# Kernel optimization log

Measured on AMD Instinct MI355X. Metric: run time of the kernel, lower is better.

The kernel has to match this reference:

```python
import math
import jax, jax.numpy as jnp
import numpy as np

# model config (matches init_kwargs)
V, D, DC, DM, DE, DG, H, L, TMAX = 32000, 1024, 512, 1024, 4096, 1024, 16, 6, 2048
CHD = max(1, DC // H)   # q/k head dim = 32
MHD = max(1, DM // H)   # v head dim   = 64
B, T = 2, 1024
EPS = 1e-5


def setup_inputs() -> dict:
    key = jax.random.key(0)
    ks = iter(jax.random.split(key, 40))
    s = 0.02
    rn = lambda shape: jax.random.normal(next(ks), shape, dtype=jnp.float32) * s
    inp = {
        'ids': jax.random.randint(next(ks), (B, T), 0, V),
        'te': rn((V, D)),            # tied token embedding / lm head weight
        'pe': rn((TMAX, D)),
        # per-layer stacked params, leading dim L
        'ln1_g': jnp.ones((L, D)), 'ln1_b': jnp.zeros((L, D)),
        'qp_w': rn((L, D, H * CHD)), 'qp_b': jnp.zeros((L, H * CHD)),
        'kp_w': rn((L, D, H * CHD)), 'kp_b': jnp.zeros((L, H * CHD)),
        'vp_w': rn((L, D, H * MHD)), 'vp_b': jnp.zeros((L, H * MHD)),
        'out_w': rn((L, H * MHD, D)), 'out_b': jnp.zeros((L, D)),
        'ln2_g': jnp.ones((L, D)), 'ln2_b': jnp.zeros((L, D)),
        'exp_w': rn((L, D, DE)), 'exp_b': jnp.zeros((L, DE)),
        'gate_w': rn((L, D, DG)), 'gate_b': jnp.zeros((L, DG)),
        'gup_w': rn((L, DG, DE)), 'gup_b': jnp.zeros((L, DE)),
        'comp_w': rn((L, DE, D)), 'comp_b': jnp.zeros((L, D)),
        'lnf_g': jnp.ones((D,)), 'lnf_b': jnp.zeros((D,)),
    }
    return inp


def _ln(x, g, b):
    m = jnp.mean(x, axis=-1, keepdims=True)
    v = jnp.mean(jnp.square(x - m), axis=-1, keepdims=True)
    return (x - m) * jax.lax.rsqrt(v + EPS) * g + b


def _forward(ids, te, pe, ln1_g, ln1_b, qp_w, qp_b, kp_w, kp_b, vp_w, vp_b,
             out_w, out_b, ln2_g, ln2_b, exp_w, exp_b, gate_w, gate_b,
             gup_w, gup_b, comp_w, comp_b, lnf_g, lnf_b):
    b, t = ids.shape
    x = te[ids] + pe[jnp.arange(t)][None, :, :]          # [B,T,D]
    causal = jnp.tril(jnp.ones((t, t), dtype=bool))       # [T,T]
    scale = 1.0 / math.sqrt(CHD)

    def block(x, p):
        (l1g, l1b, qw, qb, kw, kb, vw, vb, ow, ob,
         l2g, l2b, ew, eb, gw, gb, guw, gub, cw, cb) = p
        # --- attention sublayer ---
        h = _ln(x, l1g, l1b)
        q = (h @ qw + qb).reshape(b, t, H, CHD)
        k = (h @ kw + kb).reshape(b, t, H, CHD)
        v = (h @ vw + vb).reshape(b, t, H, MHD)
        sc = jnp.einsum('bqhd,bkhd->bhqk', q, k) * scale
        sc = jnp.where(causal[None, None], sc, -jnp.inf)
        a = jax.nn.softmax(sc, axis=-1)
        y = jnp.einsum('bhqk,bkhd->bqhd', a, v).reshape(b, t, H * MHD)
        x = x + y @ ow + ob
        # --- gated FFN sublayer ---
        h2 = _ln(x, l2g, l2b)
        e = h2 @ ew + eb
        g = jax.nn.sigmoid(jax.nn.silu(h2 @ gw + gb) @ guw + gub)
        x = x + jax.nn.silu(e * g) @ cw + cb
        return x, None

    params = (ln1_g, ln1_b, qp_w, qp_b, kp_w, kp_b, vp_w, vp_b, out_w, out_b,
              ln2_g, ln2_b, exp_w, exp_b, gate_w, gate_b, gup_w, gup_b,
              comp_w, comp_b)
    x, _ = jax.lax.scan(block, x, params)
    logits = _ln(x, lnf_g, lnf_b) @ te.T                  # tied head, [B,T,V]
    return logits


def reference(ids, te, pe, ln1_g, ln1_b, qp_w, qp_b, kp_w, kp_b, vp_w, vp_b,
              out_w, out_b, ln2_g, ln2_b, exp_w, exp_b, gate_w, gate_b,
              gup_w, gup_b, comp_w, comp_b, lnf_g, lnf_b):
    return _forward(ids, te, pe, ln1_g, ln1_b, qp_w, qp_b, kp_w, kp_b,
                    vp_w, vp_b, out_w, out_b, ln2_g, ln2_b, exp_w, exp_b,
                    gate_w, gate_b, gup_w, gup_b, comp_w, comp_b,
                    lnf_g, lnf_b)
```

## Files before the change

kernel.cpp:

```cpp
#include <hip/hip_runtime.h>
#include <math.h>

typedef unsigned short u16;
typedef unsigned int   u32;
typedef __attribute__((ext_vector_type(4))) float f32x4;
typedef __attribute__((ext_vector_type(8))) short s16x8;

#define D_   1024
#define DE_  4096
#define H_   16
#define CHD_ 32
#define MHD_ 64
#define L_   6
#define B_   2
#define T_   1024
#define M_   (B_*T_)
#define V_   32000
#define EPS_ 1e-5f

__device__ __forceinline__ float bf2f(u16 u){ return __uint_as_float(((u32)u) << 16); }
__device__ __forceinline__ u16 f2bf(float f){
    u32 x = __float_as_uint(f);
    return (u16)((x + 0x7fffu + ((x >> 16) & 1u)) >> 16);
}
__device__ __forceinline__ float ldf(const void* p, size_t i, int f16){
    return f16 ? bf2f(((const u16*)p)[i]) : ((const float*)p)[i];
}
__device__ __forceinline__ float sigf(float x){ return 1.f / (1.f + __expf(-x)); }

typedef __attribute__((address_space(3))) u32 as3_u32;
typedef const __attribute__((address_space(1))) u32 as1_u32;
__device__ __forceinline__ void gld16(const void* g, void* l){
    __builtin_amdgcn_global_load_lds((as1_u32*)g, (as3_u32*)l, 16, 0, 0);
}
__device__ __forceinline__ int swz(int row){ return (row >> 1) & 3; }

__global__ void detect_dtype(const u16* __restrict__ te_u16, int* __restrict__ flag){
    __shared__ int any_big;
    if (threadIdx.x == 0) any_big = 0;
    __syncthreads();
    int big = 0;
    #pragma unroll
    for (int i=0;i<4;i++){
        u16 u = te_u16[threadIdx.x + 256*i];
        int e = (u >> 7) & 0xFF;
        if (e >= 0x88) big = 1;
    }
    if (big) any_big = 1;
    __syncthreads();
    if (threadIdx.x == 0) *flag = any_big ? 0 : 1;
}

__global__ __launch_bounds__(256) void conv_te(const void* __restrict__ te,
        u16* __restrict__ dst, const int* __restrict__ flagp){
    int f16 = *flagp;
    size_t i = ((size_t)blockIdx.x*256 + threadIdx.x)*8;
    if (f16){
        *(s16x8*)(dst+i) = *(const s16x8*)((const u16*)te + i);
    } else {
        const float* s = (const float*)te + i;
        float4 f0 = *(const float4*)s, f1 = *(const float4*)(s+4);
        s16x8 pk;
        pk[0]=(short)f2bf(f0.x); pk[1]=(short)f2bf(f0.y);
        pk[2]=(short)f2bf(f0.z); pk[3]=(short)f2bf(f0.w);
        pk[4]=(short)f2bf(f1.x); pk[5]=(short)f2bf(f1.y);
        pk[6]=(short)f2bf(f1.z); pk[7]=(short)f2bf(f1.w);
        *(s16x8*)(dst+i) = pk;
    }
}

__global__ __launch_bounds__(256) void embed_kernel(const int* __restrict__ ids,
        const void* __restrict__ te, const void* __restrict__ pe,
        float* __restrict__ x, const int* __restrict__ flagp){
    int f16 = *flagp;
    int idx = blockIdx.x*256 + threadIdx.x;
    int m = idx >> 10, d = idx & 1023;
    int t = m & (T_-1);
    x[idx] = ldf(te, (size_t)ids[m]*D_ + d, f16) + ldf(pe, (size_t)t*D_ + d, f16);
}

__device__ __forceinline__ float blk_sum(float v, float* smem){
    #pragma unroll
    for (int o=32;o>0;o>>=1) v += __shfl_xor(v, o);
    __syncthreads();
    if ((threadIdx.x & 63) == 0) smem[threadIdx.x>>6] = v;
    __syncthreads();
    return smem[0]+smem[1]+smem[2]+smem[3];
}

__global__ __launch_bounds__(256) void ln_kernel(const float* __restrict__ x,
        const void* __restrict__ g, const void* __restrict__ b, size_t goff,
        u16* __restrict__ out, const int* __restrict__ flagp){
    __shared__ float smem[4];
    int f16 = *flagp;
    int row = blockIdx.x, tid = threadIdx.x;
    const float* xr = x + (size_t)row*D_;
    float v[4]; float s = 0.f;
    #pragma unroll
    for (int i=0;i<4;i++){ v[i] = xr[tid+256*i]; s += v[i]; }
    float mean = blk_sum(s, smem) * (1.f/D_);
    float vs = 0.f;
    #pragma unroll
    for (int i=0;i<4;i++){ float d = v[i]-mean; vs += d*d; }
    float inv = rsqrtf(blk_sum(vs, smem)*(1.f/D_) + EPS_);
    u16* orow = out + (size_t)row*D_;
    #pragma unroll
    for (int i=0;i<4;i++){
        int c = tid+256*i;
        orow[c] = f2bf((v[i]-mean)*inv*ldf(g, goff+c, f16) + ldf(b, goff+c, f16));
    }
}

__global__ __launch_bounds__(256) void wt_tr(
        const void* s0, size_t o0, u16* d0,
        const void* s1, size_t o1, u16* d1,
        const void* s2, size_t o2, u16* d2,
        int K, int N, const int* __restrict__ flagp){
    const void* s; size_t o; u16* d;
    if (blockIdx.z == 0){ s=s0; o=o0; d=d0; }
    else if (blockIdx.z == 1){ s=s1; o=o1; d=d1; }
    else { s=s2; o=o2; d=d2; }
    int f16 = *flagp;
    __shared__ float tile[64][65];
    int k0 = blockIdx.y*64, n0 = blockIdx.x*64;
    int t = threadIdx.x;
    if (!f16){
        int c4 = (t & 15)*4, r = t >> 4;
        const float* S = (const float*)s + o + (size_t)(k0 + r)*N + n0 + c4;
        #pragma unroll
        for (int i=0;i<4;i++){
            float4 v = *(const float4*)(S + (size_t)(16*i)*N);
            tile[r+16*i][c4+0] = v.x; tile[r+16*i][c4+1] = v.y;
            tile[r+16*i][c4+2] = v.z; tile[r+16*i][c4+3] = v.w;
        }
    } else {
        int c = t & 63, r4 = t >> 6;
        #pragma unroll
        for (int i=0;i<16;i++){
            int r = r4 + i*4;
            tile[r][c] = bf2f(((const u16*)s)[o + (size_t)(k0+r)*N + n0 + c]);
        }
    }
    __syncthreads();
    int n = t >> 2, kq = (t & 3)*16;
    s16x8 lo, hi;
    #pragma unroll
    for (int i=0;i<8;i++) lo[i] = (short)f2bf(tile[kq+i][n]);
    #pragma unroll
    for (int i=0;i<8;i++) hi[i] = (short)f2bf(tile[kq+8+i][n]);
    u16* D = d + (size_t)(n0+n)*K + k0 + kq;
    *(s16x8*)D = lo;
    *(s16x8*)(D+8) = hi;
}

__global__ __launch_bounds__(256) void v_transpose(const u16* __restrict__ qkv,
                                                   u16* __restrict__ vt){
    __shared__ u16 tile[32][34];
    int bh = blockIdx.z, b = bh >> 4, h = bh & 15;
    int t0 = blockIdx.x*32, d0 = blockIdx.y*32;
    int c = threadIdx.x & 31, r8 = threadIdx.x >> 5;
    #pragma unroll
    for (int i=0;i<4;i++){
        int r = r8 + i*8;
        tile[r][c] = qkv[(size_t)(b*T_ + t0 + r)*2048 + 1024 + h*64 + d0 + c];
    }
    __syncthreads();
    #pragma unroll
    for (int i=0;i<4;i++){
        int r = r8 + i*8;
        vt[(size_t)(bh*64 + d0 + r)*T_ + t0 + c] = tile[c][r];
    }
}

__global__ __launch_bounds__(256) void bias_cat(
        const void* qb_, const void* kb_, const void* vb_,
        const void* eb_, const void* gb_,
        size_t oq, size_t ok, size_t ov, size_t oe, size_t og,
        float* __restrict__ b1, float* __restrict__ b2,
        const int* __restrict__ flagp){
    int f16 = *flagp;
    int i = blockIdx.x*256 + threadIdx.x;
    if (i < 2048){
        float v = (i < 512)  ? ldf(qb_, oq + i, f16)
                : (i < 1024) ? ldf(kb_, ok + i - 512, f16)
                :              ldf(vb_, ov + i - 1024, f16);
        b1[i] = v;
    } else {
        int j = i - 2048;
        float v = (j < DE_) ? ldf(eb_, oe + j, f16)
                            : ldf(gb_, og + j - DE_, f16);
        b2[j] = v;
    }
}

template<int MODE, bool RESID, bool BIASF32, int TN, int SK>
__global__ __launch_bounds__(256) void gemm_mfma(
        const u16* __restrict__ A, int lda,
        const void* __restrict__ B, int ldb,
        const void* __restrict__ bias, size_t boff,
        void* __restrict__ C, int ldc,
        int N, int K, const int* __restrict__ flagp){
    constexpr int MT = (TN == 128) ? 4 : 2;
    constexpr int NT = 4;
    constexpr int BCALLS = TN / 32;
    __shared__ __align__(16) char smem[16384 + TN*128];
    char* ldsA = smem;
    char* ldsB = smem + 16384;
    const int t = threadIdx.x;
    const int w = t >> 6, lane = t & 63;
    const int fr = lane & 15, g = lane >> 4;
    const int wm = (TN == 128) ? (w >> 1) * 64 : w * 32;
    const int wn = (TN == 128) ? (w & 1) * 64 : 0;

    const int gx = gridDim.x, gy = gridDim.y;
    const int nwg = gx * gy;
    const int lin = blockIdx.y * gx + blockIdx.x;
    const int neu = (lin & 7) * (nwg >> 3) + (lin >> 3);
    const int m0 = (neu % gy) * 128;
    const int n0 = (neu / gy) * TN;

    const int f16 = *flagp;
    const bool convB = (MODE == 3) && !f16;

    const int srow = t >> 3, sslot = t & 7;
    const u16* srcA   = A + (size_t)(m0 + srow) * lda + 8 * (sslot ^ (srow & 7));
    const u16* srcB16 = (const u16*)B + (size_t)(n0 + srow) * ldb + 8 * (sslot ^ (srow & 7));
    const int crow = t >> 1, chalf = t & 1;
    const float* srcBf = (const float*)B + (size_t)(n0 + crow) * ldb;

    char* dstA = ldsA + w * 1024;
    char* dstB = ldsB + w * 1024;

    f32x4 acc[MT][NT];
    const f32x4 zero = {0.f, 0.f, 0.f, 0.f};
    #pragma unroll
    for (int i=0;i<MT;i++)
        #pragma unroll
        for (int j=0;j<NT;j++) acc[i][j] = zero;

    const int kps  = K / SK;
    const int kbeg = (SK > 1) ? blockIdx.z * kps : 0;
    const int kend = kbeg + kps;

    for (int k0 = kbeg; k0 < kend; k0 += 64){
        #pragma unroll
        for (int i=0;i<4;i++)
            gld16(srcA + (size_t)(32*i)*lda + k0, dstA + i*4096);
        if (!convB){
            #pragma unroll
            for (int i=0;i<BCALLS;i++)
                gld16(srcB16 + (size_t)(32*i)*ldb + k0, dstB + i*4096);
        } else {
            #pragma unroll
            for (int s4=0;s4<4;s4++){
                int sl = chalf*4 + s4;
                const float* sp = srcBf + k0 + 8*(sl ^ (crow & 7));
                float4 f0 = *(const float4*)sp;
                float4 f1 = *(const float4*)(sp + 4);
                s16x8 pk;
                pk[0]=(short)f2bf(f0.x); pk[1]=(short)f2bf(f0.y);
                pk[2]=(short)f2bf(f0.z); pk[3]=(short)f2bf(f0.w);
                pk[4]=(short)f2bf(f1.x); pk[5]=(short)f2bf(f1.y);
                pk[6]=(short)f2bf(f1.z); pk[7]=(short)f2bf(f1.w);
                *(s16x8*)(ldsB + crow*128 + sl*16) = pk;
            }
        }
        __syncthreads();
        #pragma unroll
        for (int kk=0;kk<2;kk++){
            const int so = ((kk*4 + g) ^ (fr & 7)) * 16;
            s16x8 a[MT], b[NT];
            #pragma unroll
            for (int mt=0;mt<MT;mt++)
                a[mt] = *(const s16x8*)(ldsA + (wm + mt*16 + fr)*128 + so);
            #pragma unroll
            for (int nt=0;nt<NT;nt++)
                b[nt] = *(const s16x8*)(ldsB + (wn + nt*16 + fr)*128 + so);
            #pragma unroll
            for (int mt=0;mt<MT;mt++)
                #pragma unroll
                for (int nt=0;nt<NT;nt++)
                    acc[mt][nt] = __builtin_amdgcn_mfma_f32_16x16x32_bf16(
                                      a[mt], b[nt], acc[mt][nt], 0, 0, 0);
        }
        __syncthreads();
    }

    const bool addb = (SK == 1) || (blockIdx.z == 0);
    #pragma unroll
    for (int nt=0;nt<NT;nt++){
        const int nc = n0 + wn + nt*16 + fr;
        float bv = 0.f;
        if (MODE != 3 && MODE != 5 && addb)
            bv = BIASF32 ? ((const float*)bias)[boff + nc]
                         : ldf(bias, boff + nc, f16);
        #pragma unroll
        for (int mt=0;mt<MT;mt++){
            #pragma unroll
            for (int r=0;r<4;r++){
                const int mr = m0 + wm + mt*16 + g*4 + r;
                const size_t idx = (size_t)mr * ldc + nc;
                float val = acc[mt][nt][r] + bv;
                if (MODE == 4){
                    if (nc >= DE_) val = val * sigf(val);
                    ((u16*)C)[idx] = f2bf(val);
                } else if (MODE == 2){
                    float e = bf2f(((const u16*)C)[idx]);
                    float z = e * sigf(val);
                    ((u16*)C)[idx] = f2bf(z * sigf(z));
                } else if (MODE == 3 || MODE == 5){
                    if (f16) ((u16*)C)[idx] = f2bf(val);
                    else     ((float*)C)[idx] = val;
                } else if (RESID){
                    if (SK > 1) unsafeAtomicAdd(&((float*)C)[idx], val);
                    else        ((float*)C)[idx] += val;
                } else {
                    ((u16*)C)[idx] = f2bf(val);
                }
            }
        }
    }
}

__global__ __launch_bounds__(256) void attn_mfma(const u16* __restrict__ qkv,
                                                 const u16* __restrict__ vt,
                                                 u16* __restrict__ y){
    __shared__ __align__(16) char smem[21504];
    char* ldsK = smem;
    char* ldsV = smem + 4096;
    char* ldsP = smem + 12288;

    const int qt = gridDim.x - 1 - blockIdx.x;
    const int h = blockIdx.y, b = blockIdx.z;
    const int t = threadIdx.x, w = t >> 6, lane = t & 63;
    const int fr = lane & 15, g = lane >> 4;
    const int q0 = qt * 64;
    const int qw = q0 + w * 16;
    const int bh = b * H_ + h;

    const int srow = t >> 2, sslot = t & 3;
    const u16* srcK = qkv + (size_t)(b*T_ + srow)*2048 + 512 + h*32
                      + 8 * (sslot ^ swz(srow));
    const int vrow = t >> 3, vslot = t & 7;
    const u16* srcV0 = vt + (size_t)(bh*64 + vrow)*T_      + 8 * (vslot ^ (vrow & 7));
    const u16* srcV1 = vt + (size_t)(bh*64 + 32 + vrow)*T_ + 8 * (vslot ^ (vrow & 7));

    s16x8 qf = *(const s16x8*)(qkv + (size_t)(b*T_ + qw + fr)*2048 + h*32 + g*8);

    char* pbase = ldsP + w * 2304;

    f32x4 o[4]; float m[4], l[4];
    #pragma unroll
    for (int f=0; f<4; f++) o[f] = (f32x4){0.f,0.f,0.f,0.f};
    #pragma unroll
    for (int r=0; r<4; r++){ m[r] = -3.0e38f; l[r] = 0.f; }

    const float scale = 0.17677669529663687f;
    const f32x4 zero = {0.f,0.f,0.f,0.f};

    for (int j0 = 0; j0 < q0 + 64; j0 += 64){
        __syncthreads();
        gld16(srcK + (size_t)j0*2048, ldsK + w*1024);
        gld16(srcV0 + j0,             ldsV + w*1024);
        gld16(srcV1 + j0,             ldsV + 4096 + w*1024);
        __syncthreads();
        if (j0 <= qw + 15){
            f32x4 s[4];
            #pragma unroll
            for (int f=0; f<4; f++){
                int row = f*16 + fr;
                s16x8 kf = *(const s16x8*)(ldsK + row*64 + (g ^ swz(row))*16);
                s[f] = __builtin_amdgcn_mfma_f32_16x16x32_bf16(qf, kf, zero, 0,0,0);
            }
            bool needmask = (j0 + 63 > qw);
            #pragma unroll
            for (int f=0; f<4; f++){
                int j = j0 + f*16 + fr;
                #pragma unroll
                for (int r=0; r<4; r++){
                    float sv = s[f][r] * scale;
                    if (needmask && j > qw + g*4 + r) sv = -3.0e38f;
                    s[f][r] = sv;
                }
            }
            float mx[4];
            #pragma unroll
            for (int r=0; r<4; r++)
                mx[r] = fmaxf(fmaxf(s[0][r], s[1][r]), fmaxf(s[2][r], s[3][r]));
            #pragma unroll
            for (int o2=8; o2>0; o2>>=1)
                #pragma unroll
                for (int r=0; r<4; r++) mx[r] = fmaxf(mx[r], __shfl_xor(mx[r], o2));
            float al[4];
            #pragma unroll
            for (int r=0; r<4; r++){
                float mn = fmaxf(m[r], mx[r]);
                al[r] = __expf(m[r] - mn);
                m[r] = mn;
            }
            float ps[4] = {0.f,0.f,0.f,0.f};
            #pragma unroll
            for (int f=0; f<4; f++)
                #pragma unroll
                for (int r=0; r<4; r++){
                    float p = __expf(s[f][r] - m[r]);
                    ps[r] += p;
                    *(u16*)(pbase + (g*4+r)*144 + (fr + 16*f)*2) = f2bf(p);
                }
            #pragma unroll
            for (int o2=8; o2>0; o2>>=1)
                #pragma unroll
                for (int r=0; r<4; r++) ps[r] += __shfl_xor(ps[r], o2);
            #pragma unroll
            for (int r=0; r<4; r++) l[r] = l[r]*al[r] + ps[r];
            #pragma unroll
            for (int f=0; f<4; f++)
                #pragma unroll
                for (int r=0; r<4; r++) o[f][r] *= al[r];
            #pragma unroll
            for (int kk=0; kk<2; kk++){
                s16x8 pa = *(const s16x8*)(pbase + fr*144 + kk*64 + g*16);
                #pragma unroll
                for (int f=0; f<4; f++){
                    int row = f*16 + fr;
                    s16x8 vb = *(const s16x8*)(ldsV + row*128 + (((kk*4+g) ^ (row&7))*16));
                    o[f] = __builtin_amdgcn_mfma_f32_16x16x32_bf16(pa, vb, o[f], 0,0,0);
                }
            }
        }
    }
    #pragma unroll
    for (int r=0; r<4; r++){
        float inv = 1.f / l[r];
        u16* yr = y + (size_t)(b*T_ + qw + g*4 + r)*1024 + h*64;
        #pragma unroll
        for (int f=0; f<4; f++)
            yr[fr + 16*f] = f2bf(o[f][r] * inv);
    }
}

extern "C" void kernel_launch(void* const* d_in, const int* in_sizes, int n_in,
                              void* d_out, int out_size, void* d_ws, size_t ws_size,
                              hipStream_t stream){
    const int*  ids   = (const int*) d_in[0];
    const void* te    = d_in[1];
    const void* pe    = d_in[2];
    const void* ln1_g = d_in[3];
    const void* ln1_b = d_in[4];
    const void* qp_w  = d_in[5];
    const void* qp_b  = d_in[6];
    const void* kp_w  = d_in[7];
    const void* kp_b  = d_in[8];
    const void* vp_w  = d_in[9];
    const void* vp_b  = d_in[10];
    const void* out_w = d_in[11];
    const void* out_b = d_in[12];
    const void* ln2_g = d_in[13];
    const void* ln2_b = d_in[14];
    const void* exp_w = d_in[15];
    const void* exp_b = d_in[16];
    const void* gate_w= d_in[17];
    const void* gate_b= d_in[18];
    const void* gup_w = d_in[19];
    const void* gup_b = d_in[20];
    const void* comp_w= d_in[21];
    const void* comp_b= d_in[22];
    const void* lnf_g = d_in[23];
    const void* lnf_b = d_in[24];

    char* ws = (char*)d_ws;
    int*   flag  = (int*)ws;
    float* bcat1 = (float*)(ws + 4096);
    float* bcat2 = (float*)(ws + 4096 + 8192);
    float* x     = (float*)(ws + (1u<<20));
    u16*   hb    = (u16*)  (ws + (9u<<20));
    u16*   qkvb  = (u16*)  (ws + (13u<<20));
    u16*   yb    = (u16*)  (ws + (21u<<20));
    u16*   vtb   = (u16*)  (ws + (25u<<20));
    u16*   eg1   = (u16*)  (ws + (13u<<20));
    u16*   wb    = (u16*)  (ws + (33u<<20));
    u16*   te16  = (u16*)  (ws + ((size_t)44<<20));

    const size_t need = ((size_t)44<<20) + (size_t)V_*D_*2 + (1u<<20);
    const bool pre = (ws_size >= need);

    detect_dtype<<<1, 256, 0, stream>>>((const u16*)te, flag);
    if (pre)
        conv_te<<<(V_*D_)/2048, 256, 0, stream>>>(te, te16, flag);
    embed_kernel<<<(M_*D_)/256, 256, 0, stream>>>(ids, te, pe, x, flag);

    for (int l=0; l<L_; l++){
        size_t lD = (size_t)l*D_;
        wt_tr<<<dim3(8,16,2), 256, 0, stream>>>(
            qp_w, (size_t)l*D_*512, wb,
            kp_w, (size_t)l*D_*512, wb + (size_t)512*1024,
            nullptr, 0, nullptr, 1024, 512, flag);
        wt_tr<<<dim3(16,16,2), 256, 0, stream>>>(
            vp_w,  (size_t)l*D_*1024,  wb + (size_t)1024*1024,
            out_w, (size_t)l*1024*1024, wb + (size_t)2048*1024,
            nullptr, 0, nullptr, 1024, 1024, flag);
        bias_cat<<<28, 256, 0, stream>>>(qp_b, kp_b, vp_b, exp_b, gate_b,
            (size_t)l*512, (size_t)l*512, (size_t)l*1024,
            (size_t)l*DE_, (size_t)l*1024, bcat1, bcat2, flag);

        ln_kernel<<<M_, 256, 0, stream>>>(x, ln1_g, ln1_b, lD, hb, flag);
        gemm_mfma<0,false,true,64,1><<<dim3(32,16), 256, 0, stream>>>(
            hb, 1024, wb, 1024, bcat1, 0, qkvb, 2048, 2048, 1024, flag);
        v_transpose<<<dim3(32,2,32), 256, 0, stream>>>(qkvb, vtb);
        attn_mfma<<<dim3(T_/64, H_, B_), 256, 0, stream>>>(qkvb, vtb, yb);
        gemm_mfma<0,true,false,64,2><<<dim3(16,16,2), 256, 0, stream>>>(
            yb, 1024, wb + (size_t)2048*1024, 1024,
            out_b, (size_t)l*1024, x, 1024, 1024, 1024, flag);

        wt_tr<<<dim3(64,16,1), 256, 0, stream>>>(
            exp_w, (size_t)l*D_*DE_, wb,
            nullptr,0,nullptr, nullptr,0,nullptr, 1024, 4096, flag);
        wt_tr<<<dim3(16,16,1), 256, 0, stream>>>(
            gate_w, (size_t)l*D_*1024, wb + (size_t)4096*1024,
            nullptr,0,nullptr, nullptr,0,nullptr, 1024, 1024, flag);
        ln_kernel<<<M_, 256, 0, stream>>>(x, ln2_g, ln2_b, lD, hb, flag);
        gemm_mfma<4,false,true,128,1><<<dim3(40,16), 256, 0, stream>>>(
            hb, 1024, wb, 1024, bcat2, 0, eg1, 5120, 5120, 1024, flag);
        wt_tr<<<dim3(64,16,1), 256, 0, stream>>>(
            gup_w, (size_t)l*1024*DE_, wb,
            nullptr,0,nullptr, nullptr,0,nullptr, 1024, 4096, flag);
        gemm_mfma<2,false,false,128,1><<<dim3(32,16), 256, 0, stream>>>(
            eg1 + 4096, 5120, wb, 1024,
            gup_b, (size_t)l*DE_, eg1, 5120, 4096, 1024, flag);
        wt_tr<<<dim3(16,64,1), 256, 0, stream>>>(
            comp_w, (size_t)l*DE_*1024, wb,
            nullptr,0,nullptr, nullptr,0,nullptr, 4096, 1024, flag);
        gemm_mfma<0,true,false,64,2><<<dim3(16,16,2), 256, 0, stream>>>(
            eg1, 5120, wb, 4096, comp_b, (size_t)l*1024, x, 1024, 1024, 4096, flag);
    }

    ln_kernel<<<M_, 256, 0, stream>>>(x, lnf_g, lnf_b, 0, hb, flag);
    if (pre)
        gemm_mfma<5,false,false,128,1><<<dim3(V_/128, M_/128), 256, 0, stream>>>(
            hb, 1024, te16, 1024, nullptr, 0, d_out, V_, V_, 1024, flag);
    else
        gemm_mfma<3,false,false,128,1><<<dim3(V_/128, M_/128), 256, 0, stream>>>(
            hb, 1024, te, 1024, nullptr, 0, d_out, V_, V_, 1024, flag);
}
```

Measured before the change: 2.170 ms.

## Double-buffer LDS tiles in GEMM and attention kernels with async prefetch

```diff
diff --git a/kernel.cpp b/kernel.cpp
--- a/kernel.cpp
+++ b/kernel.cpp
@@ -30,8 +30,21 @@
 
 typedef __attribute__((address_space(3))) u32 as3_u32;
 typedef const __attribute__((address_space(1))) u32 as1_u32;
+typedef __attribute__((address_space(3))) const char as3c;
 __device__ __forceinline__ void gld16(const void* g, void* l){
     __builtin_amdgcn_global_load_lds((as1_u32*)g, (as3_u32*)l, 16, 0, 0);
+}
+__device__ __forceinline__ s16x8 dsr(const char* p){
+    s16x8 v;
+    u32 off = (u32)(size_t)(as3c*)p;
+    asm volatile("ds_read_b128 %0, %1" : "=v"(v) : "v"(off));
+    return v;
+}
+#define LGKM0()  asm volatile("s_waitcnt lgkmcnt(0)" ::: "memory")
+#define SCHED0() __builtin_amdgcn_sched_barrier(0)
+#define SBAR()   __builtin_amdgcn_s_barrier()
+template<int N> __device__ __forceinline__ void vmwait(){
+    asm volatile("s_waitcnt vmcnt(%0)" :: "n"(N) : "memory");
 }
 __device__ __forceinline__ int swz(int row){ return (row >> 1) & 3; }
 
@@ -193,19 +206,28 @@
     }
 }
 
+template<int BC>
+__device__ __forceinline__ void stage_ab(const u16* sA, const u16* sB,
+        int lda, int ldb, char* dA, char* dB, int k0){
+    #pragma unroll
+    for (int i=0;i<4;i++)  gld16(sA + (size_t)(32*i)*lda + k0, dA + i*4096);
+    #pragma unroll
+    for (int i=0;i<BC;i++) gld16(sB + (size_t)(32*i)*ldb + k0, dB + i*4096);
+}
+
 template<int MODE, bool RESID, bool BIASF32, int TN, int SK>
-__global__ __launch_bounds__(256) void gemm_mfma(
+__global__ __launch_bounds__(256) void gemm_pipe(
         const u16* __restrict__ A, int lda,
-        const void* __restrict__ B, int ldb,
+        const u16* __restrict__ B, int ldb,
         const void* __restrict__ bias, size_t boff,
         void* __restrict__ C, int ldc,
         int N, int K, const int* __restrict__ flagp){
     constexpr int MT = (TN == 128) ? 4 : 2;
     constexpr int NT = 4;
-    constexpr int BCALLS = TN / 32;
-    __shared__ __align__(16) char smem[16384 + TN*128];
-    char* ldsA = smem;
-    char* ldsB = smem + 16384;
+    constexpr int BC = TN / 32;
+    constexpr int L  = 4 + BC;
+    constexpr int BUFSZ = 16384 + TN*128;
+    __shared__ __align__(16) char smem[2*BUFSZ];
     const int t = threadIdx.x;
     const int w = t >> 6, lane = t & 63;
     const int fr = lane & 15, g = lane >> 4;
@@ -220,36 +242,132 @@
     const int n0 = (neu / gy) * TN;
 
     const int f16 = *flagp;
-    const bool convB = (MODE == 3) && !f16;
 
     const int srow = t >> 3, sslot = t & 7;
-    const u16* srcA   = A + (size_t)(m0 + srow) * lda + 8 * (sslot ^ (srow & 7));
+    const u16* srcA = A + (size_t)(m0 + srow) * lda + 8 * (sslot ^ (srow & 7));
+    const u16* srcB = B + (size_t)(n0 + srow) * ldb + 8 * (sslot ^ (srow & 7));
+
+    f32x4 acc[MT][NT];
+    #pragma unroll
+    for (int i=0;i<MT;i++)
+        #pragma unroll
+        for (int j=0;j<NT;j++) acc[i][j] = (f32x4){0.f,0.f,0.f,0.f};
+
+    const int kps  = K / SK;
+    const int kbeg = (SK > 1) ? blockIdx.z * kps : 0;
+    const int nt_  = kps >> 6;
+
+    stage_ab<BC>(srcA, srcB, lda, ldb,
+                 smem + w*1024, smem + 16384 + w*1024, kbeg);
+    for (int it=0; it<nt_; ++it){
+        const int cur = it & 1;
+        if (it+1 < nt_){
+            const int nb = cur^1;
+            stage_ab<BC>(srcA, srcB, lda, ldb,
+                         smem + nb*BUFSZ + w*1024,
+                         smem + nb*BUFSZ + 16384 + w*1024,
+                         kbeg + (it+1)*64);
+            vmwait<L>();
+        } else {
+            vmwait<0>();
+        }
+        SBAR();
+        const char* bA = smem + cur*BUFSZ;
+        const char* bB = smem + cur*BUFSZ + 16384;
+        #pragma unroll
+        for (int kk=0;kk<2;kk++){
+            const int so = ((kk*4 + g) ^ (fr & 7)) * 16;
+            s16x8 a[MT], b[NT];
+            #pragma unroll
+            for (int mt=0;mt<MT;mt++)
+                a[mt] = dsr(bA + (wm + mt*16 + fr)*128 + so);
+            #pragma unroll
+            for (int n2=0;n2<NT;n2++)
+                b[n2] = dsr(bB + (wn + n2*16 + fr)*128 + so);
+            LGKM0(); SCHED0();
+            #pragma unroll
+            for (int mt=0;mt<MT;mt++)
+                #pragma unroll
+                for (int n2=0;n2<NT;n2++)
+                    acc[mt][n2] = __builtin_amdgcn_mfma_f32_16x16x32_bf16(
+                                      a[mt], b[n2], acc[mt][n2], 0, 0, 0);
+        }
+        SBAR();
+    }
+
+    const bool addb = (SK == 1) || (blockIdx.z == 0);
+    #pragma unroll
+    for (int n2=0;n2<NT;n2++){
+        const int nc = n0 + wn + n2*16 + fr;
+        float bv = 0.f;
+        if (MODE != 5 && addb)
+            bv = BIASF32 ? ((const float*)bias)[boff + nc]
+                         : ldf(bias, boff + nc, f16);
+        #pragma unroll
+        for (int mt=0;mt<MT;mt++){
+            #pragma unroll
+            for (int r=0;r<4;r++){
+                const int mr = m0 + wm + mt*16 + g*4 + r;
+                const size_t idx = (size_t)mr * ldc + nc;
+                float val = acc[mt][n2][r] + bv;
+                if (MODE == 4){
+                    if (nc >= DE_) val = val * sigf(val);
+                    ((u16*)C)[idx] = f2bf(val);
+                } else if (MODE == 2){
+                    float e = bf2f(((const u16*)C)[idx]);
+                    float z = e * sigf(val);
+                    ((u16*)C)[idx] = f2bf(z * sigf(z));
+                } else if (MODE == 5){
+                    if (f16) ((u16*)C)[idx] = f2bf(val);
+                    else     ((float*)C)[idx] = val;
+                } else if (RESID){
+                    if (SK > 1) unsafeAtomicAdd(&((float*)C)[idx], val);
+                    else        ((float*)C)[idx] += val;
+                } else {
+                    ((u16*)C)[idx] = f2bf(val);
+                }
+            }
+        }
+    }
+}
+
+__global__ __launch_bounds__(256) void gemm_head_f32(
+        const u16* __restrict__ A, int lda,
+        const void* __restrict__ B, int ldb,
+        void* __restrict__ C, int ldc,
+        int N, int K, const int* __restrict__ flagp){
+    __shared__ __align__(16) char smem[16384 + 16384];
+    char* ldsA = smem;
+    char* ldsB = smem + 16384;
+    const int t = threadIdx.x;
+    const int w = t >> 6, lane = t & 63;
+    const int fr = lane & 15, g = lane >> 4;
+    const int wm = (w >> 1) * 64, wn = (w & 1) * 64;
+    const int gx = gridDim.x, gy = gridDim.y;
+    const int nwg = gx * gy;
+    const int lin = blockIdx.y * gx + blockIdx.x;
+    const int neu = (lin & 7) * (nwg >> 3) + (lin >> 3);
+    const int m0 = (neu % gy) * 128;
+    const int n0 = (neu / gy) * 128;
+    const int f16 = *flagp;
+    const int srow = t >> 3, sslot = t & 7;
+    const u16* srcA = A + (size_t)(m0 + srow) * lda + 8 * (sslot ^ (srow & 7));
     const u16* srcB16 = (const u16*)B + (size_t)(n0 + srow) * ldb + 8 * (sslot ^ (srow & 7));
     const int crow = t >> 1, chalf = t & 1;
     const float* srcBf = (const float*)B + (size_t)(n0 + crow) * ldb;
-
-    char* dstA = ldsA + w * 1024;
-    char* dstB = ldsB + w * 1024;
-
-    f32x4 acc[MT][NT];
-    const f32x4 zero = {0.f, 0.f, 0.f, 0.f};
-    #pragma unroll
-    for (int i=0;i<MT;i++)
-        #pragma unroll
-        for (int j=0;j<NT;j++) acc[i][j] = zero;
-
-    const int kps  = K / SK;
-    const int kbeg = (SK > 1) ? blockIdx.z * kps : 0;
-    const int kend = kbeg + kps;
-
-    for (int k0 = kbeg; k0 < kend; k0 += 64){
+    f32x4 acc[4][4];
+    #pragma unroll
+    for (int i=0;i<4;i++)
+        #pragma unroll
+        for (int j=0;j<4;j++) acc[i][j] = (f32x4){0.f,0.f,0.f,0.f};
+    for (int k0 = 0; k0 < K; k0 += 64){
         #pragma unroll
         for (int i=0;i<4;i++)
-            gld16(srcA + (size_t)(32*i)*lda + k0, dstA + i*4096);
-        if (!convB){
-            #pragma unroll
-            for (int i=0;i<BCALLS;i++)
-                gld16(srcB16 + (size_t)(32*i)*ldb + k0, dstB + i*4096);
+            gld16(srcA + (size_t)(32*i)*lda + k0, ldsA + w*1024 + i*4096);
+        if (f16){
+            #pragma unroll
+            for (int i=0;i<4;i++)
+                gld16(srcB16 + (size_t)(32*i)*ldb + k0, ldsB + w*1024 + i*4096);
         } else {
             #pragma unroll
             for (int s4=0;s4<4;s4++){
@@ -269,54 +387,33 @@
         #pragma unroll
         for (int kk=0;kk<2;kk++){
             const int so = ((kk*4 + g) ^ (fr & 7)) * 16;
-            s16x8 a[MT], b[NT];
-            #pragma unroll
-            for (int mt=0;mt<MT;mt++)
+            s16x8 a[4], b[4];
+            #pragma unroll
+            for (int mt=0;mt<4;mt++)
                 a[mt] = *(const s16x8*)(ldsA + (wm + mt*16 + fr)*128 + so);
             #pragma unroll
-            for (int nt=0;nt<NT;nt++)
+            for (int nt=0;nt<4;nt++)
                 b[nt] = *(const s16x8*)(ldsB + (wn + nt*16 + fr)*128 + so);
             #pragma unroll
-            for (int mt=0;mt<MT;mt++)
-                #pragma unroll
-                for (int nt=0;nt<NT;nt++)
+            for (int mt=0;mt<4;mt++)
+                #pragma unroll
+                for (int nt=0;nt<4;nt++)
                     acc[mt][nt] = __builtin_amdgcn_mfma_f32_16x16x32_bf16(
                                       a[mt], b[nt], acc[mt][nt], 0, 0, 0);
         }
         __syncthreads();
     }
-
-    const bool addb = (SK == 1) || (blockIdx.z == 0);
-    #pragma unroll
-    for (int nt=0;nt<NT;nt++){
+    #pragma unroll
+    for (int nt=0;nt<4;nt++){
         const int nc = n0 + wn + nt*16 + fr;
-        float bv = 0.f;
-        if (MODE != 3 && MODE != 5 && addb)
-            bv = BIASF32 ? ((const float*)bias)[boff + nc]
-                         : ldf(bias, boff + nc, f16);
-        #pragma unroll
-        for (int mt=0;mt<MT;mt++){
+        #pragma unroll
+        for (int mt=0;mt<4;mt++){
             #pragma unroll
             for (int r=0;r<4;r++){
                 const int mr = m0 + wm + mt*16 + g*4 + r;
                 const size_t idx = (size_t)mr * ldc + nc;
-                float val = acc[mt][nt][r] + bv;
-                if (MODE == 4){
-                    if (nc >= DE_) val = val * sigf(val);
-                    ((u16*)C)[idx] = f2bf(val);
-                } else if (MODE == 2){
-                    float e = bf2f(((const u16*)C)[idx]);
-                    float z = e * sigf(val);
-                    ((u16*)C)[idx] = f2bf(z * sigf(z));
-                } else if (MODE == 3 || MODE == 5){
-                    if (f16) ((u16*)C)[idx] = f2bf(val);
-                    else     ((float*)C)[idx] = val;
-                } else if (RESID){
-                    if (SK > 1) unsafeAtomicAdd(&((float*)C)[idx], val);
-                    else        ((float*)C)[idx] += val;
-                } else {
-                    ((u16*)C)[idx] = f2bf(val);
-                }
+                if (f16) ((u16*)C)[idx] = f2bf(acc[mt][nt][r]);
+                else     ((float*)C)[idx] = acc[mt][nt][r];
             }
         }
     }
@@ -325,10 +422,10 @@
 __global__ __launch_bounds__(256) void attn_mfma(const u16* __restrict__ qkv,
                                                  const u16* __restrict__ vt,
                                                  u16* __restrict__ y){
-    __shared__ __align__(16) char smem[21504];
+    __shared__ __align__(16) char smem[33792];
     char* ldsK = smem;
-    char* ldsV = smem + 4096;
-    char* ldsP = smem + 12288;
+    char* ldsV = smem + 8192;
+    char* ldsP = smem + 24576;
 
     const int qt = gridDim.x - 1 - blockIdx.x;
     const int h = blockIdx.y, b = blockIdx.z;
@@ -358,20 +455,39 @@
     const float scale = 0.17677669529663687f;
     const f32x4 zero = {0.f,0.f,0.f,0.f};
 
-    for (int j0 = 0; j0 < q0 + 64; j0 += 64){
-        __syncthreads();
-        gld16(srcK + (size_t)j0*2048, ldsK + w*1024);
-        gld16(srcV0 + j0,             ldsV + w*1024);
-        gld16(srcV1 + j0,             ldsV + 4096 + w*1024);
-        __syncthreads();
-        if (j0 <= qw + 15){
+    gld16(srcK,      ldsK + w*1024);
+    gld16(srcV0,     ldsV + w*1024);
+    gld16(srcV1,     ldsV + 4096 + w*1024);
+
+    const int ntt = qt + 1;
+    for (int it = 0; it < ntt; ++it){
+        const int cur = it & 1;
+        if (it+1 < ntt){
+            const int nb = cur^1;
+            const int j1 = (it+1)*64;
+            gld16(srcK + (size_t)j1*2048, ldsK + nb*4096 + w*1024);
+            gld16(srcV0 + j1,             ldsV + nb*8192 + w*1024);
+            gld16(srcV1 + j1,             ldsV + nb*8192 + 4096 + w*1024);
+            vmwait<3>();
+        } else {
+            vmwait<0>();
+        }
+        SBAR();
+        const int j0 = it*64;
+        const char* bK = ldsK + cur*4096;
+        const char* bV = ldsV + cur*8192;
+        {
             f32x4 s[4];
+            s16x8 kfr[4];
             #pragma unroll
             for (int f=0; f<4; f++){
                 int row = f*16 + fr;
-                s16x8 kf = *(const s16x8*)(ldsK + row*64 + (g ^ swz(row))*16);
-                s[f] = __builtin_amdgcn_mfma_f32_16x16x32_bf16(qf, kf, zero, 0,0,0);
+                kfr[f] = dsr(bK + row*64 + (g ^ swz(row))*16);
             }
+            LGKM0(); SCHED0();
+            #pragma unroll
+            for (int f=0; f<4; f++)
+                s[f] = __builtin_amdgcn_mfma_f32_16x16x32_bf16(qf, kfr[f], zero, 0,0,0);
             bool needmask = (j0 + 63 > qw);
             #pragma unroll
             for (int f=0; f<4; f++){
@@ -420,14 +536,19 @@
             #pragma unroll
             for (int kk=0; kk<2; kk++){
                 s16x8 pa = *(const s16x8*)(pbase + fr*144 + kk*64 + g*16);
+                s16x8 vbr[4];
                 #pragma unroll
                 for (int f=0; f<4; f++){
                     int row = f*16 + fr;
-                    s16x8 vb = *(const s16x8*)(ldsV + row*128 + (((kk*4+g) ^ (row&7))*16));
-                    o[f] = __builtin_amdgcn_mfma_f32_16x16x32_bf16(pa, vb, o[f], 0,0,0);
+                    vbr[f] = dsr(bV + row*128 + (((kk*4+g) ^ (row&7))*16));
                 }
+                LGKM0(); SCHED0();
+                #pragma unroll
+                for (int f=0; f<4; f++)
+                    o[f] = __builtin_amdgcn_mfma_f32_16x16x32_bf16(pa, vbr[f], o[f], 0,0,0);
             }
         }
+        SBAR();
     }
     #pragma unroll
     for (int r=0; r<4; r++){
@@ -504,11 +625,11 @@
             (size_t)l*DE_, (size_t)l*1024, bcat1, bcat2, flag);
 
         ln_kernel<<<M_, 256, 0, stream>>>(x, ln1_g, ln1_b, lD, hb, flag);
-        gemm_mfma<0,false,true,64,1><<<dim3(32,16), 256, 0, stream>>>(
+        gemm_pipe<0,false,true,64,1><<<dim3(32,16), 256, 0, stream>>>(
             hb, 1024, wb, 1024, bcat1, 0, qkvb, 2048, 2048, 1024, flag);
         v_transpose<<<dim3(32,2,32), 256, 0, stream>>>(qkvb, vtb);
         attn_mfma<<<dim3(T_/64, H_, B_), 256, 0, stream>>>(qkvb, vtb, yb);
-        gemm_mfma<0,true,false,64,2><<<dim3(16,16,2), 256, 0, stream>>>(
+        gemm_pipe<0,true,false,64,2><<<dim3(16,16,2), 256, 0, stream>>>(
             yb, 1024, wb + (size_t)2048*1024, 1024,
             out_b, (size_t)l*1024, x, 1024, 1024, 1024, flag);
 
@@ -519,26 +640,26 @@
             gate_w, (size_t)l*D_*1024, wb + (size_t)4096*1024,
             nullptr,0,nullptr, nullptr,0,nullptr, 1024, 1024, flag);
         ln_kernel<<<M_, 256, 0, stream>>>(x, ln2_g, ln2_b, lD, hb, flag);
-        gemm_mfma<4,false,true,128,1><<<dim3(40,16), 256, 0, stream>>>(
+        gemm_pipe<4,false,true,128,1><<<dim3(40,16), 256, 0, stream>>>(
             hb, 1024, wb, 1024, bcat2, 0, eg1, 5120, 5120, 1024, flag);
         wt_tr<<<dim3(64,16,1), 256, 0, stream>>>(
             gup_w, (size_t)l*1024*DE_, wb,
             nullptr,0,nullptr, nullptr,0,nullptr, 1024, 4096, flag);
-        gemm_mfma<2,false,false,128,1><<<dim3(32,16), 256, 0, stream>>>(
+        gemm_pipe<2,false,false,128,1><<<dim3(32,16), 256, 0, stream>>>(
             eg1 + 4096, 5120, wb, 1024,
             gup_b, (size_t)l*DE_, eg1, 5120, 4096, 1024, flag);
         wt_tr<<<dim3(16,64,1), 256, 0, stream>>>(
             comp_w, (size_t)l*DE_*1024, wb,
             nullptr,0,nullptr, nullptr,0,nullptr, 4096, 1024, flag);
-        gemm_mfma<0,true,false,64,2><<<dim3(16,16,2), 256, 0, stream>>>(
+        gemm_pipe<0,true,false,64,2><<<dim3(16,16,2), 256, 0, stream>>>(
             eg1, 5120, wb, 4096, comp_b, (size_t)l*1024, x, 1024, 1024, 4096, flag);
     }
 
     ln_kernel<<<M_, 256, 0, stream>>>(x, lnf_g, lnf_b, 0, hb, flag);
     if (pre)
-        gemm_mfma<5,false,false,128,1><<<dim3(V_/128, M_/128), 256, 0, stream>>>(
+        gemm_pipe<5,false,false,128,1><<<dim3(V_/128, M_/128), 256, 0, stream>>>(
             hb, 1024, te16, 1024, nullptr, 0, d_out, V_, V_, 1024, flag);
     else
-        gemm_mfma<3,false,false,128,1><<<dim3(V_/128, M_/128), 256, 0, stream>>>(
-            hb, 1024, te, 1024, nullptr, 0, d_out, V_, V_, 1024, flag);
-}
+        gemm_head_f32<<<dim3(V_/128, M_/128), 256, 0, stream>>>(
+            hb, 1024, te, 1024, d_out, V_, V_, 1024, flag);
+}
```

New measurement: 2.026 ms. 6.6% less time.
